# Optimization experiments

Hardware: AMD Instinct MI355X
Metric: run time of the kernel (lower is better)

Reference implementation:

```python
import jax, jax.numpy as jnp
import numpy as np

N_STATE = 1280
N_HEAD = 20
D_HEAD = N_STATE // N_HEAD  # 64
N_MLP = 4 * N_STATE         # 5120
EPS = 1e-5


def _layer_norm(x, gamma, beta):
    mu = jnp.mean(x, axis=-1, keepdims=True)
    var = jnp.mean(jnp.square(x - mu), axis=-1, keepdims=True)
    return (x - mu) * jax.lax.rsqrt(var + EPS) * gamma + beta


def setup_inputs() -> dict:
    key = jax.random.key(0)
    ks = jax.random.split(key, 16)
    s = lambda fan_in: 1.0 / np.sqrt(fan_in)
    d = {
        "x": jax.random.normal(ks[0], (1, 1500, N_STATE), jnp.float32),
        # attention projections (stored [in, out]; torch Linear does x @ W.T + b)
        "Wq": jax.random.normal(ks[1], (N_STATE, N_STATE), jnp.float32) * s(N_STATE),
        "bq": jax.random.normal(ks[2], (N_STATE,), jnp.float32) * 0.02,
        "Wk": jax.random.normal(ks[3], (N_STATE, N_STATE), jnp.float32) * s(N_STATE),  # no bias
        "Wv": jax.random.normal(ks[4], (N_STATE, N_STATE), jnp.float32) * s(N_STATE),
        "bv": jax.random.normal(ks[5], (N_STATE,), jnp.float32) * 0.02,
        "Wo": jax.random.normal(ks[6], (N_STATE, N_STATE), jnp.float32) * s(N_STATE),
        "bo": jax.random.normal(ks[7], (N_STATE,), jnp.float32) * 0.02,
        # layer norms
        "ln1_g": jnp.ones((N_STATE,), jnp.float32),
        "ln1_b": jnp.zeros((N_STATE,), jnp.float32),
        "ln2_g": jnp.ones((N_STATE,), jnp.float32),
        "ln2_b": jnp.zeros((N_STATE,), jnp.float32),
        # MLP
        "W1": jax.random.normal(ks[8], (N_STATE, N_MLP), jnp.float32) * s(N_STATE),
        "b1": jax.random.normal(ks[9], (N_MLP,), jnp.float32) * 0.02,
        "W2": jax.random.normal(ks[10], (N_MLP, N_STATE), jnp.float32) * s(N_MLP),
        "b2": jax.random.normal(ks[11], (N_STATE,), jnp.float32) * 0.02,
    }
    return d


def reference(x, Wq, bq, Wk, Wv, bv, Wo, bo, ln1_g, ln1_b, ln2_g, ln2_b, W1, b1, W2, b2):
    B, S, C = x.shape
    scale = D_HEAD ** -0.5

    # --- multi-head self-attention ---
    h = _layer_norm(x, ln1_g, ln1_b)
    q = (h @ Wq + bq).reshape(B, S, N_HEAD, D_HEAD)
    k = (h @ Wk).reshape(B, S, N_HEAD, D_HEAD)
    v = (h @ Wv + bv).reshape(B, S, N_HEAD, D_HEAD)
    # scores: [B, H, Q, K]; softmax over keys (dim=1 'k' in the torch einsum)
    scores = jnp.einsum('bqhd,bkhd->bhqk', q, k) * scale
    w = jax.nn.softmax(scores, axis=-1)
    attn = jnp.einsum('bhqk,bkhd->bqhd', w, v).reshape(B, S, C)
    attn = attn @ Wo + bo
    x = x + attn

    # --- MLP (exact GELU, matching torch nn.GELU default) ---
    h2 = _layer_norm(x, ln2_g, ln2_b)
    h2 = jax.nn.gelu(h2 @ W1 + b1, approximate=False)
    x = x + (h2 @ W2 + b2)
    return x
```

## Files before the change

kernel.cpp:

```cpp
#include <hip/hip_runtime.h>
#include <hip/hip_bf16.h>
#include <math.h>

typedef __bf16 bf16x8 __attribute__((ext_vector_type(8)));
typedef float f32x4 __attribute__((ext_vector_type(4)));

#define SEQ 1500
#define CDIM 1280
#define NHEAD 20
#define DHEAD 64
#define NMLP 5120
#define QKVN 3840
#define VTLD 1504
#define APAD 68

#define GLOAD_LDS16(gp, lp)                                                    \
  __builtin_amdgcn_global_load_lds(                                            \
      (const __attribute__((address_space(1))) unsigned int*)(gp),             \
      (__attribute__((address_space(3))) unsigned int*)(lp), 16, 0, 0)

__global__ __launch_bounds__(256) void pack_params_kernel(
    const unsigned int* __restrict__ xw, const void* bq, const void* bv,
    const void* bo, const void* g1, const void* be1, const void* g2,
    const void* be2, const void* b1, const void* b2,
    __bf16* __restrict__ pb, int* __restrict__ flag) {
  __shared__ int cnt[256];
  const unsigned int w = xw[threadIdx.x];
  const unsigned int e = (w >> 7) & 0xFF;
  cnt[threadIdx.x] = (e >= 100 && e <= 150) ? 1 : 0;
  __syncthreads();
  for (int s = 128; s > 0; s >>= 1) {
    if (threadIdx.x < (unsigned)s) cnt[threadIdx.x] += cnt[threadIdx.x + s];
    __syncthreads();
  }
  const int isbf = (cnt[0] >= 160) ? 1 : 0;
  if (blockIdx.x == 0 && threadIdx.x == 0) flag[0] = isbf;
  const int i = blockIdx.x * 256 + threadIdx.x;
  if (i >= 16640) return;
  auto ld = [&](const void* p, int j) -> float {
    return isbf ? (float)((const __bf16*)p)[j] : ((const float*)p)[j];
  };
  float v;
  if (i < 3840) {
    if (i < 1280) v = ld(bq, i);
    else if (i < 2560) v = 0.f;
    else v = ld(bv, i - 2560);
  } else if (i < 5120) v = ld(bo, i - 3840);
  else if (i < 6400) v = ld(g1, i - 5120);
  else if (i < 7680) v = ld(be1, i - 6400);
  else if (i < 8960) v = ld(g2, i - 7680);
  else if (i < 10240) v = ld(be2, i - 8960);
  else if (i < 15360) v = ld(b1, i - 10240);
  else v = ld(b2, i - 15360);
  pb[i] = (__bf16)v;
}

__device__ __forceinline__ void transpose_body(const void* in, __bf16* out,
                                               int K, int N, int isbf,
                                               int bx, int by) {
  __shared__ __bf16 t[32][33];
  const int tx = threadIdx.x, ty = threadIdx.y;
  const int n0 = bx * 32, k0 = by * 32;
  if (isbf) {
    const __bf16* s = (const __bf16*)in;
#pragma unroll
    for (int i = ty; i < 32; i += 8)
      t[i][tx] = s[(size_t)(k0 + i) * N + n0 + tx];
  } else {
    const float* s = (const float*)in;
#pragma unroll
    for (int i = ty; i < 32; i += 8)
      t[i][tx] = (__bf16)s[(size_t)(k0 + i) * N + n0 + tx];
  }
  __syncthreads();
#pragma unroll
  for (int i = ty; i < 32; i += 8)
    out[(size_t)(n0 + i) * K + k0 + tx] = t[tx][i];
}

__global__ __launch_bounds__(256) void transpose_all_kernel(
    const void* Wq, const void* Wk, const void* Wv, const void* Wo,
    const void* W1, const void* W2, __bf16* __restrict__ Wqkvt,
    __bf16* __restrict__ Wot, __bf16* __restrict__ W1t,
    __bf16* __restrict__ W2t, const int* __restrict__ flag) {
  const int id = blockIdx.x;
  const int isbf = flag[0];
  if (id < 6400) {
    const int w = id / 1600, r = id % 1600;
    const void* in = (w == 0) ? Wq : (w == 1) ? Wk : (w == 2) ? Wv : Wo;
    __bf16* out = (w < 3) ? (Wqkvt + (size_t)w * CDIM * CDIM) : Wot;
    transpose_body(in, out, CDIM, CDIM, isbf, r % 40, r / 40);
  } else if (id < 12800) {
    const int r = id - 6400;
    transpose_body(W1, W1t, CDIM, NMLP, isbf, r % 160, r / 160);
  } else {
    const int r = id - 12800;
    transpose_body(W2, W2t, NMLP, CDIM, isbf, r % 40, r / 40);
  }
}

__global__ __launch_bounds__(256) void transpose_act_kernel(const __bf16* __restrict__ in,
                                                            __bf16* __restrict__ out,
                                                            int istride) {
  __shared__ __bf16 t[32][33];
  const int tx = threadIdx.x, ty = threadIdx.y;
  const int n0 = blockIdx.x * 32, k0 = blockIdx.y * 32;
#pragma unroll
  for (int i = ty; i < 32; i += 8) {
    const int k = k0 + i;
    t[i][tx] = (k < SEQ) ? in[(size_t)k * istride + n0 + tx] : (__bf16)0.f;
  }
  __syncthreads();
#pragma unroll
  for (int i = ty; i < 32; i += 8) {
    const int kk = k0 + tx;
    if (kk < VTLD) out[(size_t)(n0 + i) * VTLD + kk] = t[tx][i];
  }
}

__global__ __launch_bounds__(256) void ln_kernel(const void* __restrict__ X,
                                                 const __bf16* __restrict__ gamma,
                                                 const __bf16* __restrict__ beta,
                                                 __bf16* __restrict__ Y,
                                                 const int* __restrict__ flag) {
  const int isf32 = (flag[0] == 0);
  const int row = blockIdx.x;
  float v[5];
  float s = 0.f, s2 = 0.f;
#pragma unroll
  for (int i = 0; i < 5; ++i) {
    const int c = threadIdx.x + 256 * i;
    const size_t idx = (size_t)row * CDIM + c;
    v[i] = isf32 ? ((const float*)X)[idx] : (float)((const __bf16*)X)[idx];
    s += v[i];
    s2 += v[i] * v[i];
  }
  const int lane = threadIdx.x & 63, wv = threadIdx.x >> 6;
#pragma unroll
  for (int off = 32; off > 0; off >>= 1) {
    s += __shfl_down(s, off);
    s2 += __shfl_down(s2, off);
  }
  __shared__ float red[8];
  if (lane == 0) { red[wv] = s; red[4 + wv] = s2; }
  __syncthreads();
  s = red[0] + red[1] + red[2] + red[3];
  s2 = red[4] + red[5] + red[6] + red[7];
  const float mu = s * (1.f / CDIM);
  const float var = s2 * (1.f / CDIM) - mu * mu;
  const float rstd = rsqrtf(fmaxf(var, 0.f) + 1e-5f);
#pragma unroll
  for (int i = 0; i < 5; ++i) {
    const int c = threadIdx.x + 256 * i;
    Y[(size_t)row * CDIM + c] =
        (__bf16)((v[i] - mu) * rstd * (float)gamma[c] + (float)beta[c]);
  }
}

__global__ __launch_bounds__(256) void resid_ln_kernel(
    const float* __restrict__ P, const __bf16* __restrict__ bo,
    const void* __restrict__ X, const __bf16* __restrict__ gamma,
    const __bf16* __restrict__ beta, __bf16* __restrict__ X1,
    __bf16* __restrict__ H2, const int* __restrict__ flag) {
  const int isf32 = (flag[0] == 0);
  const int row = blockIdx.x;
  const int MN = SEQ * CDIM;
  float v[5];
  float s = 0.f, s2 = 0.f;
#pragma unroll
  for (int i = 0; i < 5; ++i) {
    const int c = threadIdx.x + 256 * i;
    const size_t idx = (size_t)row * CDIM + c;
    const float xv = isf32 ? ((const float*)X)[idx] : (float)((const __bf16*)X)[idx];
    const float val = P[idx] + P[MN + idx] + (float)bo[c] + xv;
    X1[idx] = (__bf16)val;
    v[i] = val;
    s += val;
    s2 += val * val;
  }
  const int lane = threadIdx.x & 63, wv = threadIdx.x >> 6;
#pragma unroll
  for (int off = 32; off > 0; off >>= 1) {
    s += __shfl_down(s, off);
    s2 += __shfl_down(s2, off);
  }
  __shared__ float red[8];
  if (lane == 0) { red[wv] = s; red[4 + wv] = s2; }
  __syncthreads();
  s = red[0] + red[1] + red[2] + red[3];
  s2 = red[4] + red[5] + red[6] + red[7];
  const float mu = s * (1.f / CDIM);
  const float var = s2 * (1.f / CDIM) - mu * mu;
  const float rstd = rsqrtf(fmaxf(var, 0.f) + 1e-5f);
#pragma unroll
  for (int i = 0; i < 5; ++i) {
    const int c = threadIdx.x + 256 * i;
    H2[(size_t)row * CDIM + c] =
        (__bf16)((v[i] - mu) * rstd * (float)gamma[c] + (float)beta[c]);
  }
}

__global__ __launch_bounds__(256) void gemm64_kernel(
    const __bf16* __restrict__ A, const __bf16* __restrict__ Bt,
    const __bf16* __restrict__ bias, void* __restrict__ Cv,
    int M, int N, int K, int KS, int gelu, int nsplit) {
  __shared__ __bf16 As[2][64 * 32];
  __shared__ __bf16 Bs[2][128 * 32];
  const int bm = blockIdx.x, bn = blockIdx.y, sz = blockIdx.z;
  const int tid = threadIdx.x;
  const int lane = tid & 63, wave = tid >> 6;
  const int l16 = lane & 15, kq = (lane >> 4) << 3;
  const int lrow = lane >> 2, lcol = (lane & 3) << 3;
  const int wn = wave * 32;

  f32x4 acc[4][2];
  const f32x4 zero = {0.f, 0.f, 0.f, 0.f};
#pragma unroll
  for (int i = 0; i < 4; ++i)
#pragma unroll
    for (int j = 0; j < 2; ++j) acc[i][j] = zero;

  const int kbeg = sz * KS;
  int kend = kbeg + KS;
  if (kend > K) kend = K;

  int ga = bm * 64 + wave * 16 + lrow;
  if (ga > M - 1) ga = M - 1;
  const __bf16* Ap = A + (size_t)ga * K + lcol;

  for (int k0 = kbeg; k0 < kend; k0 += 64) {
#pragma unroll
    for (int c = 0; c < 2; ++c)
      GLOAD_LDS16(Ap + k0 + c * 32, &As[c][wave * 512]);
#pragma unroll
    for (int c = 0; c < 2; ++c)
#pragma unroll
      for (int t = 0; t < 2; ++t) {
        const int seg = t * 4 + wave;
        const int gb = bn * 128 + seg * 16 + lrow;
        GLOAD_LDS16(Bt + (size_t)gb * K + k0 + c * 32 + lcol, &Bs[c][seg * 512]);
      }
    __syncthreads();
    bf16x8 af[4][2], bfr[2][2];
#pragma unroll
    for (int i = 0; i < 4; ++i)
#pragma unroll
      for (int c = 0; c < 2; ++c)
        af[i][c] = *(const bf16x8*)(&As[c][(i * 16 + l16) * 32 + kq]);
#pragma unroll
    for (int j = 0; j < 2; ++j)
#pragma unroll
      for (int c = 0; c < 2; ++c)
        bfr[j][c] = *(const bf16x8*)(&Bs[c][(wn + j * 16 + l16) * 32 + kq]);
#pragma unroll
    for (int i = 0; i < 4; ++i)
#pragma unroll
      for (int j = 0; j < 2; ++j)
#pragma unroll
        for (int c = 0; c < 2; ++c)
          acc[i][j] = __builtin_amdgcn_mfma_f32_16x16x32_bf16(af[i][c], bfr[j][c],
                                                              acc[i][j], 0, 0, 0);
    __syncthreads();
  }

  const int rq4 = (lane >> 4) * 4;
  if (nsplit > 1) {
    float* P = (float*)Cv + (size_t)sz * M * N;
#pragma unroll
    for (int i = 0; i < 4; ++i)
#pragma unroll
      for (int r = 0; r < 4; ++r) {
        const int grow = bm * 64 + i * 16 + rq4 + r;
        if (grow >= M) continue;
#pragma unroll
        for (int j = 0; j < 2; ++j) {
          const int gcol = bn * 128 + wn + j * 16 + l16;
          P[(size_t)grow * N + gcol] = acc[i][j][r];
        }
      }
  } else {
    __bf16* Cb = (__bf16*)Cv;
#pragma unroll
    for (int i = 0; i < 4; ++i)
#pragma unroll
      for (int r = 0; r < 4; ++r) {
        const int grow = bm * 64 + i * 16 + rq4 + r;
        if (grow >= M) continue;
#pragma unroll
        for (int j = 0; j < 2; ++j) {
          const int gcol = bn * 128 + wn + j * 16 + l16;
          float vv = acc[i][j][r];
          if (bias) vv += (float)bias[gcol];
          if (gelu) vv = 0.5f * vv * (1.f + erff(vv * 0.70710678118654752f));
          Cb[(size_t)grow * N + gcol] = (__bf16)vv;
        }
      }
  }
}

__global__ __launch_bounds__(256) void gemm128s_kernel(
    const __bf16* __restrict__ A, const __bf16* __restrict__ Bt,
    const __bf16* __restrict__ bias, __bf16* __restrict__ C,
    int M, int N, int K, int gelu, int mtiles) {
  __shared__ __bf16 As[2][2][128 * 32];
  __shared__ __bf16 Bs[2][2][128 * 32];

  const int id = blockIdx.x;
  const int xcd = id & 7;
  const int grp = id >> 3;
  const int bm = grp % mtiles;
  const int bn = (grp / mtiles) * 8 + xcd;
  if (bn >= (N >> 7)) return;

  const int tid = threadIdx.x;
  const int lane = tid & 63, wave = tid >> 6;
  const int wm = (wave >> 1) * 64, wn = (wave & 1) * 64;
  const int l16 = lane & 15, kq = (lane >> 4) << 3;
  const int lrow = lane >> 2, lcol = (lane & 3) << 3;

  f32x4 acc[4][4];
  const f32x4 zero = {0.f, 0.f, 0.f, 0.f};
#pragma unroll
  for (int i = 0; i < 4; ++i)
#pragma unroll
    for (int j = 0; j < 4; ++j) acc[i][j] = zero;

  const __bf16* Ap[2];
  const __bf16* Bp[2];
#pragma unroll
  for (int t = 0; t < 2; ++t) {
    int ga = bm * 128 + t * 64 + wave * 16 + lrow;
    if (ga > M - 1) ga = M - 1;
    Ap[t] = A + (size_t)ga * K + lcol;
    const int gb = bn * 128 + t * 64 + wave * 16 + lrow;
    Bp[t] = Bt + (size_t)gb * K + lcol;
  }

  auto stage = [&](int b, int k0) {
#pragma unroll
    for (int t = 0; t < 2; ++t)
#pragma unroll
      for (int c = 0; c < 2; ++c) {
        GLOAD_LDS16(Ap[t] + k0 + c * 32, &As[b][c][(t * 64 + wave * 16) * 32]);
        GLOAD_LDS16(Bp[t] + k0 + c * 32, &Bs[b][c][(t * 64 + wave * 16) * 32]);
      }
  };

  stage(0, 0);
  int buf = 0;
  for (int k0 = 0; k0 < K; k0 += 64) {
    __syncthreads();
    if (k0 + 64 < K) stage(buf ^ 1, k0 + 64);
    bf16x8 af[4][2], bfr[4][2];
#pragma unroll
    for (int i = 0; i < 4; ++i)
#pragma unroll
      for (int c = 0; c < 2; ++c)
        af[i][c] = *(const bf16x8*)(&As[buf][c][(wm + i * 16 + l16) * 32 + kq]);
#pragma unroll
    for (int j = 0; j < 4; ++j)
#pragma unroll
      for (int c = 0; c < 2; ++c)
        bfr[j][c] = *(const bf16x8*)(&Bs[buf][c][(wn + j * 16 + l16) * 32 + kq]);
#pragma unroll
    for (int i = 0; i < 4; ++i)
#pragma unroll
      for (int j = 0; j < 4; ++j)
#pragma unroll
        for (int c = 0; c < 2; ++c)
          acc[i][j] = __builtin_amdgcn_mfma_f32_16x16x32_bf16(af[i][c], bfr[j][c],
                                                              acc[i][j], 0, 0, 0);
    buf ^= 1;
  }

  const int rq4 = (lane >> 4) * 4;
#pragma unroll
  for (int i = 0; i < 4; ++i)
#pragma unroll
    for (int r = 0; r < 4; ++r) {
      const int grow = bm * 128 + wm + i * 16 + rq4 + r;
      if (grow >= M) continue;
#pragma unroll
      for (int j = 0; j < 4; ++j) {
        const int gcol = bn * 128 + wn + j * 16 + l16;
        float vv = acc[i][j][r];
        if (bias) vv += (float)bias[gcol];
        if (gelu) vv = 0.5f * vv * (1.f + erff(vv * 0.70710678118654752f));
        C[(size_t)grow * N + gcol] = (__bf16)vv;
      }
    }
}

__global__ __launch_bounds__(256) void reduce_kernel(
    const float* __restrict__ P, const __bf16* __restrict__ bias,
    const __bf16* __restrict__ resid, void* __restrict__ out,
    int MN, int N, const int* __restrict__ flag) {
  const int i = blockIdx.x * 256 + threadIdx.x;
  if (i >= MN) return;
  const float v = P[i] + P[(size_t)MN + i] + (float)bias[i % N] + (float)resid[i];
  if (flag[0]) ((__bf16*)out)[i] = (__bf16)v;
  else         ((float*)out)[i] = v;
}

__global__ __launch_bounds__(256) void attn_mfma_kernel(
    const __bf16* __restrict__ Q,
    const __bf16* __restrict__ Kk,
    const __bf16* __restrict__ Vt,
    float* __restrict__ Opart,
    float* __restrict__ ml,
    int rs) {
  const int h = blockIdx.y;
  const int q0 = blockIdx.x * 64;
  const int z = blockIdx.z;
  const int tid = threadIdx.x;
  const int wave = tid >> 6, lane = tid & 63;
  const int l16 = lane & 15, quad = lane >> 4;

  __shared__ __bf16 Ks[64 * APAD];
  __shared__ __bf16 Vs[64 * APAD];
  __shared__ __bf16 Ps[4][16 * APAD];

  bf16x8 qf[2];
  {
    int q = q0 + wave * 16 + l16;
    if (q > SEQ - 1) q = SEQ - 1;
    const __bf16* qp = Q + (size_t)q * rs + h * DHEAD + quad * 8;
    qf[0] = *(const bf16x8*)(qp);
    qf[1] = *(const bf16x8*)(qp + 32);
  }

  f32x4 oacc[4];
  const f32x4 zero = {0.f, 0.f, 0.f, 0.f};
#pragma unroll
  for (int jt = 0; jt < 4; ++jt) oacc[jt] = zero;
  float mrow[4], lrow[4];
#pragma unroll
  for (int r = 0; r < 4; ++r) { mrow[r] = -30000.f; lrow[r] = 0.f; }

  const int srow = tid >> 2;
  const int scol = (tid & 3) << 4;

  const __bf16* Kbase = Kk + h * DHEAD;
  const __bf16* Vbase = Vt + (size_t)(h * DHEAD + srow) * VTLD;

  for (int kt = z * 12; kt < z * 12 + 12; ++kt) {
    const int key0 = kt * 64;
    __syncthreads();
    {
      int gk = key0 + srow;
      if (gk > SEQ - 1) gk = SEQ - 1;
      const __bf16* kp = Kbase + (size_t)gk * rs + scol;
      *(bf16x8*)(&Ks[srow * APAD + scol]) = *(const bf16x8*)(kp);
      *(bf16x8*)(&Ks[srow * APAD + scol + 8]) = *(const bf16x8*)(kp + 8);
      const __bf16* vp = Vbase + key0 + scol;
      *(bf16x8*)(&Vs[srow * APAD + scol]) = *(const bf16x8*)(vp);
      *(bf16x8*)(&Vs[srow * APAD + scol + 8]) = *(const bf16x8*)(vp + 8);
    }
    __syncthreads();

    f32x4 s[4];
#pragma unroll
    for (int jt = 0; jt < 4; ++jt) s[jt] = zero;
#pragma unroll
    for (int jt = 0; jt < 4; ++jt)
#pragma unroll
      for (int ks = 0; ks < 2; ++ks) {
        const bf16x8 kf = *(const bf16x8*)(&Ks[(jt * 16 + l16) * APAD + ks * 32 + quad * 8]);
        s[jt] = __builtin_amdgcn_mfma_f32_16x16x32_bf16(qf[ks], kf, s[jt], 0, 0, 0);
      }

#pragma unroll
    for (int jt = 0; jt < 4; ++jt) {
      const int key = key0 + jt * 16 + l16;
#pragma unroll
      for (int r = 0; r < 4; ++r) {
        float sv = s[jt][r] * 0.125f;
        if (key >= SEQ) sv = -30000.f;
        s[jt][r] = sv;
      }
    }

#pragma unroll
    for (int r = 0; r < 4; ++r) {
      float tmax = fmaxf(fmaxf(s[0][r], s[1][r]), fmaxf(s[2][r], s[3][r]));
#pragma unroll
      for (int off = 8; off > 0; off >>= 1) tmax = fmaxf(tmax, __shfl_xor(tmax, off));
      const float mnew = fmaxf(mrow[r], tmax);
      const float alpha = __expf(mrow[r] - mnew);
      mrow[r] = mnew;
      lrow[r] *= alpha;
#pragma unroll
      for (int jt = 0; jt < 4; ++jt) oacc[jt][r] *= alpha;
#pragma unroll
      for (int jt = 0; jt < 4; ++jt) {
        const float p = __expf(s[jt][r] - mnew);
        lrow[r] += p;
        Ps[wave][(quad * 4 + r) * APAD + jt * 16 + l16] = (__bf16)p;
      }
    }

    bf16x8 pf[2];
    pf[0] = *(const bf16x8*)(&Ps[wave][l16 * APAD + quad * 8]);
    pf[1] = *(const bf16x8*)(&Ps[wave][l16 * APAD + 32 + quad * 8]);
#pragma unroll
    for (int jt = 0; jt < 4; ++jt)
#pragma unroll
      for (int ks = 0; ks < 2; ++ks) {
        const bf16x8 vf = *(const bf16x8*)(&Vs[(jt * 16 + l16) * APAD + ks * 32 + quad * 8]);
        oacc[jt] = __builtin_amdgcn_mfma_f32_16x16x32_bf16(pf[ks], vf, oacc[jt], 0, 0, 0);
      }
  }

  float* Oz = Opart + (size_t)z * SEQ * CDIM;
#pragma unroll
  for (int r = 0; r < 4; ++r) {
    float lt = lrow[r];
#pragma unroll
    for (int off = 8; off > 0; off >>= 1) lt += __shfl_xor(lt, off);
    const int q = q0 + wave * 16 + quad * 4 + r;
    if (q < SEQ) {
#pragma unroll
      for (int jt = 0; jt < 4; ++jt)
        Oz[(size_t)q * CDIM + h * DHEAD + jt * 16 + l16] = oacc[jt][r];
      if (l16 == 0) {
        const size_t mi = ((size_t)(z * NHEAD + h) * SEQ + q) * 2;
        ml[mi] = mrow[r];
        ml[mi + 1] = lt;
      }
    }
  }
}

__global__ __launch_bounds__(256) void attn_combine_kernel(
    const float* __restrict__ Op, const float* __restrict__ ml,
    __bf16* __restrict__ O) {
  const int i = blockIdx.x * 256 + threadIdx.x;
  if (i >= SEQ * CDIM) return;
  const int q = i / CDIM;
  const int h = (i % CDIM) >> 6;
  const size_t m1i = ((size_t)h * SEQ + q) * 2;
  const size_t m2i = ((size_t)(NHEAD + h) * SEQ + q) * 2;
  const float m1 = ml[m1i], l1 = ml[m1i + 1];
  const float m2 = ml[m2i], l2 = ml[m2i + 1];
  const float M = fmaxf(m1, m2);
  const float e1 = __expf(m1 - M), e2 = __expf(m2 - M);
  const float v = (e1 * Op[i] + e2 * Op[(size_t)SEQ * CDIM + i]) /
                  (e1 * l1 + e2 * l2);
  O[i] = (__bf16)v;
}

extern "C" void kernel_launch(void* const* d_in, const int* in_sizes, int n_in,
                              void* d_out, int out_size, void* d_ws, size_t ws_size,
                              hipStream_t stream) {
  const void* x   = d_in[0];
  const void* Wq  = d_in[1];
  const void* bq  = d_in[2];
  const void* Wk  = d_in[3];
  const void* Wv  = d_in[4];
  const void* bv  = d_in[5];
  const void* Wo  = d_in[6];
  const void* bo  = d_in[7];
  const void* g1  = d_in[8];
  const void* be1 = d_in[9];
  const void* g2  = d_in[10];
  const void* be2 = d_in[11];
  const void* W1  = d_in[12];
  const void* bm1 = d_in[13];
  const void* W2  = d_in[14];
  const void* bm2 = d_in[15];

  char* ws = (char*)d_ws;
  size_t off = 0;
  auto alloc = [&](size_t elems) {
    __bf16* p = (__bf16*)(ws + off);
    off += elems * sizeof(__bf16);
    return p;
  };
  __bf16* Wqkvt = alloc((size_t)QKVN * CDIM);
  __bf16* Wot   = alloc((size_t)CDIM * CDIM);
  __bf16* W1t   = alloc((size_t)CDIM * NMLP);
  __bf16* W2t   = alloc((size_t)CDIM * NMLP);
  __bf16* qkvb  = alloc((size_t)SEQ * QKVN);
  __bf16* hb    = alloc((size_t)SEQ * CDIM);
  __bf16* mb    = alloc((size_t)SEQ * NMLP);
  __bf16* pb    = alloc(20480);
  off = (off + 15) & ~(size_t)15;
  float* pscr = (float*)(ws + off);
  off += (size_t)2 * SEQ * CDIM * sizeof(float);
  float* mlb = (float*)(ws + off);
  off += (size_t)2 * NHEAD * SEQ * 2 * sizeof(float);
  int* flag = (int*)(ws + off);

  __bf16* vtb  = mb;
  __bf16* x1b  = qkvb;
  __bf16* h2b  = qkvb + (size_t)SEQ * CDIM;

  __bf16* qkvbias = pb + 0;
  __bf16* bo_b  = pb + 3840;
  __bf16* g1_b  = pb + 5120;
  __bf16* be1_b = pb + 6400;
  __bf16* g2_b  = pb + 7680;
  __bf16* be2_b = pb + 8960;
  __bf16* b1_b  = pb + 10240;
  __bf16* b2_b  = pb + 15360;

  pack_params_kernel<<<65, 256, 0, stream>>>(
      (const unsigned int*)x, bq, bv, bo, g1, be1, g2, be2, bm1, bm2, pb, flag);
  transpose_all_kernel<<<19200, dim3(32, 8), 0, stream>>>(
      Wq, Wk, Wv, Wo, W1, W2, Wqkvt, Wot, W1t, W2t, flag);
  ln_kernel<<<SEQ, 256, 0, stream>>>(x, g1_b, be1_b, hb, flag);
  gemm64_kernel<<<dim3(24, 30, 1), 256, 0, stream>>>(
      hb, Wqkvt, qkvbias, qkvb, SEQ, QKVN, CDIM, CDIM, 0, 1);
  transpose_act_kernel<<<dim3(40, 47), dim3(32, 8), 0, stream>>>(
      qkvb + 2560, vtb, QKVN);
  attn_mfma_kernel<<<dim3(24, NHEAD, 2), 256, 0, stream>>>(
      qkvb, qkvb + 1280, vtb, pscr, mlb, QKVN);
  attn_combine_kernel<<<7500, 256, 0, stream>>>(pscr, mlb, hb);
  gemm64_kernel<<<dim3(24, 10, 2), 256, 0, stream>>>(
      hb, Wot, nullptr, pscr, SEQ, CDIM, CDIM, 640, 0, 2);
  resid_ln_kernel<<<SEQ, 256, 0, stream>>>(pscr, bo_b, x, g2_b, be2_b,
                                           x1b, h2b, flag);
  gemm128s_kernel<<<12 * 40, 256, 0, stream>>>(
      h2b, W1t, b1_b, mb, SEQ, NMLP, CDIM, 1, 12);
  gemm64_kernel<<<dim3(24, 10, 2), 256, 0, stream>>>(
      mb, W2t, nullptr, pscr, SEQ, CDIM, NMLP, 2560, 0, 2);
  reduce_kernel<<<7500, 256, 0, stream>>>(pscr, b2_b, x1b, d_out,
                                          SEQ * CDIM, CDIM, flag);
}
```

Measured before the change: 365.2 us.

## Replace 128x128 GEMM with 8-wave 128x256 ping-pong kernel for QKV and MLP1

```diff
diff --git a/kernel.cpp b/kernel.cpp
--- a/kernel.cpp
+++ b/kernel.cpp
@@ -298,25 +298,47 @@
   }
 }
 
-__global__ __launch_bounds__(256) void gemm128s_kernel(
+__global__ __launch_bounds__(512, 2) void gemm8ph_kernel(
     const __bf16* __restrict__ A, const __bf16* __restrict__ Bt,
     const __bf16* __restrict__ bias, __bf16* __restrict__ C,
     int M, int N, int K, int gelu, int mtiles) {
-  __shared__ __bf16 As[2][2][128 * 32];
-  __shared__ __bf16 Bs[2][2][128 * 32];
-
-  const int id = blockIdx.x;
-  const int xcd = id & 7;
-  const int grp = id >> 3;
-  const int bm = grp % mtiles;
-  const int bn = (grp / mtiles) * 8 + xcd;
-  if (bn >= (N >> 7)) return;
+  __shared__ __bf16 As[2][128 * 64];
+  __shared__ __bf16 Bs[2][256 * 64];
+
+  const int nwg = mtiles * (N >> 8);
+  const int qq = nwg >> 3, rr = nwg & 7;
+  const int xcd = blockIdx.x & 7, rk = blockIdx.x >> 3;
+  const int wg = (xcd < rr ? xcd * (qq + 1) : rr * (qq + 1) + (xcd - rr) * qq) + rk;
+  const int bm = wg % mtiles, bn = wg / mtiles;
 
   const int tid = threadIdx.x;
   const int lane = tid & 63, wave = tid >> 6;
-  const int wm = (wave >> 1) * 64, wn = (wave & 1) * 64;
-  const int l16 = lane & 15, kq = (lane >> 4) << 3;
-  const int lrow = lane >> 2, lcol = (lane & 3) << 3;
+  const int wm = wave >> 2, wn = wave & 3;
+  const int l16 = lane & 15, quad = lane >> 4;
+
+  const int rA = tid >> 3;
+  const int sl = tid & 7;
+  const int aoff = ((sl * 16) ^ ((rA & 7) << 4)) >> 1;
+  int gm0 = bm * 128 + rA;        if (gm0 > M - 1) gm0 = M - 1;
+  int gm1 = bm * 128 + 64 + rA;   if (gm1 > M - 1) gm1 = M - 1;
+  const __bf16* ApA = A + (size_t)gm0 * K + aoff;
+  const __bf16* ApB = A + (size_t)gm1 * K + aoff;
+  const __bf16* Bp[4];
+#pragma unroll
+  for (int L = 0; L < 4; ++L)
+    Bp[L] = Bt + (size_t)(bn * 256 + L * 64 + rA) * K + aoff;
+
+  auto stage = [&](int b, int k0) {
+    GLOAD_LDS16(ApA + k0, &As[b][(size_t)tid * 8]);
+    GLOAD_LDS16(ApB + k0, &As[b][4096 + (size_t)tid * 8]);
+#pragma unroll
+    for (int L = 0; L < 4; ++L)
+      GLOAD_LDS16(Bp[L] + k0, &Bs[b][L * 4096 + (size_t)tid * 8]);
+  };
+
+  const int xsw = (l16 & 7) << 4;
+  const int kb0 = (((quad << 4)) ^ xsw) >> 1;
+  const int kb1 = (((quad << 4) + 64) ^ xsw) >> 1;
 
   f32x4 acc[4][4];
   const f32x4 zero = {0.f, 0.f, 0.f, 0.f};
@@ -325,64 +347,75 @@
 #pragma unroll
     for (int j = 0; j < 4; ++j) acc[i][j] = zero;
 
-  const __bf16* Ap[2];
-  const __bf16* Bp[2];
-#pragma unroll
-  for (int t = 0; t < 2; ++t) {
-    int ga = bm * 128 + t * 64 + wave * 16 + lrow;
-    if (ga > M - 1) ga = M - 1;
-    Ap[t] = A + (size_t)ga * K + lcol;
-    const int gb = bn * 128 + t * 64 + wave * 16 + lrow;
-    Bp[t] = Bt + (size_t)gb * K + lcol;
-  }
-
-  auto stage = [&](int b, int k0) {
-#pragma unroll
-    for (int t = 0; t < 2; ++t)
-#pragma unroll
-      for (int c = 0; c < 2; ++c) {
-        GLOAD_LDS16(Ap[t] + k0 + c * 32, &As[b][c][(t * 64 + wave * 16) * 32]);
-        GLOAD_LDS16(Bp[t] + k0 + c * 32, &Bs[b][c][(t * 64 + wave * 16) * 32]);
-      }
-  };
-
+  const int NT = K >> 6;
   stage(0, 0);
-  int buf = 0;
-  for (int k0 = 0; k0 < K; k0 += 64) {
-    __syncthreads();
-    if (k0 + 64 < K) stage(buf ^ 1, k0 + 64);
-    bf16x8 af[4][2], bfr[4][2];
+  asm volatile("s_waitcnt vmcnt(0)" ::: "memory");
+  __builtin_amdgcn_sched_barrier(0);
+  __builtin_amdgcn_s_barrier();
+
+  bf16x8 af[4][2], bfr[4][2];
+  for (int t = 0; t < NT; ++t) {
+    const int cur = t & 1;
+#pragma unroll
+    for (int i = 0; i < 4; ++i) {
+      const int row = wm * 64 + i * 16 + l16;
+      af[i][0] = *(const bf16x8*)(&As[cur][row * 64 + kb0]);
+      af[i][1] = *(const bf16x8*)(&As[cur][row * 64 + kb1]);
+    }
+#pragma unroll
+    for (int j = 0; j < 2; ++j) {
+      const int row = wn * 64 + j * 16 + l16;
+      bfr[j][0] = *(const bf16x8*)(&Bs[cur][row * 64 + kb0]);
+      bfr[j][1] = *(const bf16x8*)(&Bs[cur][row * 64 + kb1]);
+    }
+    if (t + 1 < NT) stage(cur ^ 1, (t + 1) * 64);
+    __builtin_amdgcn_s_barrier();
+    asm volatile("s_waitcnt lgkmcnt(0)" ::: "memory");
+    __builtin_amdgcn_sched_barrier(0);
+    __builtin_amdgcn_s_setprio(1);
 #pragma unroll
     for (int i = 0; i < 4; ++i)
 #pragma unroll
-      for (int c = 0; c < 2; ++c)
-        af[i][c] = *(const bf16x8*)(&As[buf][c][(wm + i * 16 + l16) * 32 + kq]);
-#pragma unroll
-    for (int j = 0; j < 4; ++j)
-#pragma unroll
-      for (int c = 0; c < 2; ++c)
-        bfr[j][c] = *(const bf16x8*)(&Bs[buf][c][(wn + j * 16 + l16) * 32 + kq]);
-#pragma unroll
-    for (int i = 0; i < 4; ++i)
-#pragma unroll
-      for (int j = 0; j < 4; ++j)
+      for (int j = 0; j < 2; ++j)
 #pragma unroll
         for (int c = 0; c < 2; ++c)
           acc[i][j] = __builtin_amdgcn_mfma_f32_16x16x32_bf16(af[i][c], bfr[j][c],
                                                               acc[i][j], 0, 0, 0);
-    buf ^= 1;
-  }
-
-  const int rq4 = (lane >> 4) * 4;
+    __builtin_amdgcn_s_setprio(0);
+    __builtin_amdgcn_s_barrier();
+#pragma unroll
+    for (int j = 2; j < 4; ++j) {
+      const int row = wn * 64 + j * 16 + l16;
+      bfr[j][0] = *(const bf16x8*)(&Bs[cur][row * 64 + kb0]);
+      bfr[j][1] = *(const bf16x8*)(&Bs[cur][row * 64 + kb1]);
+    }
+    __builtin_amdgcn_s_barrier();
+    asm volatile("s_waitcnt lgkmcnt(0)" ::: "memory");
+    __builtin_amdgcn_sched_barrier(0);
+    __builtin_amdgcn_s_setprio(1);
+#pragma unroll
+    for (int i = 0; i < 4; ++i)
+#pragma unroll
+      for (int j = 2; j < 4; ++j)
+#pragma unroll
+        for (int c = 0; c < 2; ++c)
+          acc[i][j] = __builtin_amdgcn_mfma_f32_16x16x32_bf16(af[i][c], bfr[j][c],
+                                                              acc[i][j], 0, 0, 0);
+    __builtin_amdgcn_s_setprio(0);
+    asm volatile("s_waitcnt vmcnt(0)" ::: "memory");
+    __builtin_amdgcn_sched_barrier(0);
+    __builtin_amdgcn_s_barrier();
+  }
+
 #pragma unroll
   for (int i = 0; i < 4; ++i)
 #pragma unroll
     for (int r = 0; r < 4; ++r) {
-      const int grow = bm * 128 + wm + i * 16 + rq4 + r;
+      const int grow = bm * 128 + wm * 64 + i * 16 + quad * 4 + r;
       if (grow >= M) continue;
 #pragma unroll
       for (int j = 0; j < 4; ++j) {
-        const int gcol = bn * 128 + wn + j * 16 + l16;
+        const int gcol = bn * 256 + wn * 64 + j * 16 + l16;
         float vv = acc[i][j][r];
         if (bias) vv += (float)bias[gcol];
         if (gelu) vv = 0.5f * vv * (1.f + erff(vv * 0.70710678118654752f));
@@ -609,8 +642,8 @@
   transpose_all_kernel<<<19200, dim3(32, 8), 0, stream>>>(
       Wq, Wk, Wv, Wo, W1, W2, Wqkvt, Wot, W1t, W2t, flag);
   ln_kernel<<<SEQ, 256, 0, stream>>>(x, g1_b, be1_b, hb, flag);
-  gemm64_kernel<<<dim3(24, 30, 1), 256, 0, stream>>>(
-      hb, Wqkvt, qkvbias, qkvb, SEQ, QKVN, CDIM, CDIM, 0, 1);
+  gemm8ph_kernel<<<180, 512, 0, stream>>>(
+      hb, Wqkvt, qkvbias, qkvb, SEQ, QKVN, CDIM, 0, 12);
   transpose_act_kernel<<<dim3(40, 47), dim3(32, 8), 0, stream>>>(
       qkvb + 2560, vtb, QKVN);
   attn_mfma_kernel<<<dim3(24, NHEAD, 2), 256, 0, stream>>>(
@@ -620,7 +653,7 @@
       hb, Wot, nullptr, pscr, SEQ, CDIM, CDIM, 640, 0, 2);
   resid_ln_kernel<<<SEQ, 256, 0, stream>>>(pscr, bo_b, x, g2_b, be2_b,
                                            x1b, h2b, flag);
-  gemm128s_kernel<<<12 * 40, 256, 0, stream>>>(
+  gemm8ph_kernel<<<240, 512, 0, stream>>>(
       h2b, W1t, b1_b, mb, SEQ, NMLP, CDIM, 1, 12);
   gemm64_kernel<<<dim3(24, 10, 2), 256, 0, stream>>>(
       mb, W2t, nullptr, pscr, SEQ, CDIM, NMLP, 2560, 0, 2);
```

New measurement: 370.5 us. Within noise of the previous version (+1.4%).

## Replace QKV and FC1 GEMMs with 64x256 tile kernel loading B into registers

Applied to the files above, without the earlier changes.

```diff
diff --git a/kernel.cpp b/kernel.cpp
--- a/kernel.cpp
+++ b/kernel.cpp
@@ -298,25 +298,37 @@
   }
 }
 
-__global__ __launch_bounds__(256) void gemm128s_kernel(
+__global__ __launch_bounds__(256, 2) void gemmbg_kernel(
     const __bf16* __restrict__ A, const __bf16* __restrict__ Bt,
     const __bf16* __restrict__ bias, __bf16* __restrict__ C,
     int M, int N, int K, int gelu, int mtiles) {
-  __shared__ __bf16 As[2][2][128 * 32];
-  __shared__ __bf16 Bs[2][2][128 * 32];
-
-  const int id = blockIdx.x;
-  const int xcd = id & 7;
-  const int grp = id >> 3;
-  const int bm = grp % mtiles;
-  const int bn = (grp / mtiles) * 8 + xcd;
-  if (bn >= (N >> 7)) return;
+  __shared__ __bf16 As[2][64 * 64];
+
+  const int nwg = mtiles * (N >> 8);
+  const int qq = nwg >> 3, rr = nwg & 7;
+  const int xcd = blockIdx.x & 7, rk = blockIdx.x >> 3;
+  const int wg = (xcd < rr ? xcd * (qq + 1) : rr * (qq + 1) + (xcd - rr) * qq) + rk;
+  const int bm = wg % mtiles, bn = wg / mtiles;
 
   const int tid = threadIdx.x;
   const int lane = tid & 63, wave = tid >> 6;
-  const int wm = (wave >> 1) * 64, wn = (wave & 1) * 64;
-  const int l16 = lane & 15, kq = (lane >> 4) << 3;
-  const int lrow = lane >> 2, lcol = (lane & 3) << 3;
+  const int l16 = lane & 15, quad = lane >> 4;
+
+  const int rA = tid >> 3, sl = tid & 7;
+  const int aswz = ((sl * 16) ^ ((rA & 7) << 4)) >> 1;
+  int gm0 = bm * 64 + rA;      if (gm0 > M - 1) gm0 = M - 1;
+  int gm1 = bm * 64 + 32 + rA; if (gm1 > M - 1) gm1 = M - 1;
+  const __bf16* Ap0 = A + (size_t)gm0 * K + aswz;
+  const __bf16* Ap1 = A + (size_t)gm1 * K + aswz;
+
+  const __bf16* Bp[4];
+#pragma unroll
+  for (int j = 0; j < 4; ++j)
+    Bp[j] = Bt + (size_t)(bn * 256 + wave * 64 + j * 16 + l16) * K + quad * 8;
+
+  const int xsw = (l16 & 7) << 4;
+  const int kb0 = ((quad * 16) ^ xsw) >> 1;
+  const int kb1 = ((64 + quad * 16) ^ xsw) >> 1;
 
   f32x4 acc[4][4];
   const f32x4 zero = {0.f, 0.f, 0.f, 0.f};
@@ -325,64 +337,67 @@
 #pragma unroll
     for (int j = 0; j < 4; ++j) acc[i][j] = zero;
 
-  const __bf16* Ap[2];
-  const __bf16* Bp[2];
-#pragma unroll
-  for (int t = 0; t < 2; ++t) {
-    int ga = bm * 128 + t * 64 + wave * 16 + lrow;
-    if (ga > M - 1) ga = M - 1;
-    Ap[t] = A + (size_t)ga * K + lcol;
-    const int gb = bn * 128 + t * 64 + wave * 16 + lrow;
-    Bp[t] = Bt + (size_t)gb * K + lcol;
-  }
-
-  auto stage = [&](int b, int k0) {
-#pragma unroll
-    for (int t = 0; t < 2; ++t)
-#pragma unroll
-      for (int c = 0; c < 2; ++c) {
-        GLOAD_LDS16(Ap[t] + k0 + c * 32, &As[b][c][(t * 64 + wave * 16) * 32]);
-        GLOAD_LDS16(Bp[t] + k0 + c * 32, &Bs[b][c][(t * 64 + wave * 16) * 32]);
-      }
-  };
-
-  stage(0, 0);
-  int buf = 0;
-  for (int k0 = 0; k0 < K; k0 += 64) {
+  const int NT = K >> 6;
+
+#define STAGE_A(b, k0)                                  \
+  do {                                                  \
+    GLOAD_LDS16(Ap0 + (k0), &As[b][tid * 8]);           \
+    GLOAD_LDS16(Ap1 + (k0), &As[b][2048 + tid * 8]);    \
+  } while (0)
+
+#define LOAD_B(bf, k0)                                  \
+  do {                                                  \
+    _Pragma("unroll")                                   \
+    for (int j = 0; j < 4; ++j) {                       \
+      bf[j][0] = *(const bf16x8*)(Bp[j] + (k0));        \
+      bf[j][1] = *(const bf16x8*)(Bp[j] + (k0) + 32);   \
+    }                                                   \
+  } while (0)
+
+#define COMPUTE(b, bf)                                                        \
+  do {                                                                        \
+    bf16x8 af[4][2];                                                          \
+    _Pragma("unroll")                                                         \
+    for (int i = 0; i < 4; ++i) {                                             \
+      const int rb = (i * 16 + l16) * 64;                                     \
+      af[i][0] = *(const bf16x8*)(&As[b][rb + kb0]);                          \
+      af[i][1] = *(const bf16x8*)(&As[b][rb + kb1]);                          \
+    }                                                                         \
+    _Pragma("unroll")                                                         \
+    for (int i = 0; i < 4; ++i)                                               \
+      _Pragma("unroll")                                                       \
+      for (int j = 0; j < 4; ++j) {                                           \
+        acc[i][j] = __builtin_amdgcn_mfma_f32_16x16x32_bf16(af[i][0], bf[j][0],\
+                                                            acc[i][j], 0, 0, 0);\
+        acc[i][j] = __builtin_amdgcn_mfma_f32_16x16x32_bf16(af[i][1], bf[j][1],\
+                                                            acc[i][j], 0, 0, 0);\
+      }                                                                       \
+  } while (0)
+
+  bf16x8 bA[4][2], bB[4][2];
+  STAGE_A(0, 0);
+  LOAD_B(bA, 0);
+  for (int t = 0; t < NT; t += 2) {
     __syncthreads();
-    if (k0 + 64 < K) stage(buf ^ 1, k0 + 64);
-    bf16x8 af[4][2], bfr[4][2];
-#pragma unroll
-    for (int i = 0; i < 4; ++i)
-#pragma unroll
-      for (int c = 0; c < 2; ++c)
-        af[i][c] = *(const bf16x8*)(&As[buf][c][(wm + i * 16 + l16) * 32 + kq]);
-#pragma unroll
-    for (int j = 0; j < 4; ++j)
-#pragma unroll
-      for (int c = 0; c < 2; ++c)
-        bfr[j][c] = *(const bf16x8*)(&Bs[buf][c][(wn + j * 16 + l16) * 32 + kq]);
-#pragma unroll
-    for (int i = 0; i < 4; ++i)
-#pragma unroll
-      for (int j = 0; j < 4; ++j)
-#pragma unroll
-        for (int c = 0; c < 2; ++c)
-          acc[i][j] = __builtin_amdgcn_mfma_f32_16x16x32_bf16(af[i][c], bfr[j][c],
-                                                              acc[i][j], 0, 0, 0);
-    buf ^= 1;
-  }
-
-  const int rq4 = (lane >> 4) * 4;
+    if (t + 1 < NT) { STAGE_A(1, (t + 1) * 64); LOAD_B(bB, (t + 1) * 64); }
+    COMPUTE(0, bA);
+    __syncthreads();
+    if (t + 2 < NT) { STAGE_A(0, (t + 2) * 64); LOAD_B(bA, (t + 2) * 64); }
+    COMPUTE(1, bB);
+  }
+#undef STAGE_A
+#undef LOAD_B
+#undef COMPUTE
+
 #pragma unroll
   for (int i = 0; i < 4; ++i)
 #pragma unroll
     for (int r = 0; r < 4; ++r) {
-      const int grow = bm * 128 + wm + i * 16 + rq4 + r;
+      const int grow = bm * 64 + i * 16 + quad * 4 + r;
       if (grow >= M) continue;
 #pragma unroll
       for (int j = 0; j < 4; ++j) {
-        const int gcol = bn * 128 + wn + j * 16 + l16;
+        const int gcol = bn * 256 + wave * 64 + j * 16 + l16;
         float vv = acc[i][j][r];
         if (bias) vv += (float)bias[gcol];
         if (gelu) vv = 0.5f * vv * (1.f + erff(vv * 0.70710678118654752f));
@@ -609,8 +624,8 @@
   transpose_all_kernel<<<19200, dim3(32, 8), 0, stream>>>(
       Wq, Wk, Wv, Wo, W1, W2, Wqkvt, Wot, W1t, W2t, flag);
   ln_kernel<<<SEQ, 256, 0, stream>>>(x, g1_b, be1_b, hb, flag);
-  gemm64_kernel<<<dim3(24, 30, 1), 256, 0, stream>>>(
-      hb, Wqkvt, qkvbias, qkvb, SEQ, QKVN, CDIM, CDIM, 0, 1);
+  gemmbg_kernel<<<360, 256, 0, stream>>>(
+      hb, Wqkvt, qkvbias, qkvb, SEQ, QKVN, CDIM, 0, 24);
   transpose_act_kernel<<<dim3(40, 47), dim3(32, 8), 0, stream>>>(
       qkvb + 2560, vtb, QKVN);
   attn_mfma_kernel<<<dim3(24, NHEAD, 2), 256, 0, stream>>>(
@@ -620,8 +635,8 @@
       hb, Wot, nullptr, pscr, SEQ, CDIM, CDIM, 640, 0, 2);
   resid_ln_kernel<<<SEQ, 256, 0, stream>>>(pscr, bo_b, x, g2_b, be2_b,
                                            x1b, h2b, flag);
-  gemm128s_kernel<<<12 * 40, 256, 0, stream>>>(
-      h2b, W1t, b1_b, mb, SEQ, NMLP, CDIM, 1, 12);
+  gemmbg_kernel<<<480, 256, 0, stream>>>(
+      h2b, W1t, b1_b, mb, SEQ, NMLP, CDIM, 1, 24);
   gemm64_kernel<<<dim3(24, 10, 2), 256, 0, stream>>>(
       mb, W2t, nullptr, pscr, SEQ, CDIM, NMLP, 2560, 0, 2);
   reduce_kernel<<<7500, 256, 0, stream>>>(pscr, b2_b, x1b, d_out,
```

New measurement: 405.4 us. 1.11x slower.
